# Optimization experiments

Hardware: AMD Instinct MI355X
Metric: run time of the kernel (lower is better)

The kernel has to match this reference:

```python
import jax, jax.numpy as jnp
import numpy as np

D_MODEL = 1024
NHEAD = 16
D_K = D_MODEL // NHEAD
EPS = 1e-5


def _layernorm(x, scale, bias):
    m = jnp.mean(x, axis=-1, keepdims=True)
    v = jnp.var(x, axis=-1, keepdims=True)
    return (x - m) * jax.lax.rsqrt(v + EPS) * scale + bias


def setup_inputs() -> dict:
    key = jax.random.key(0)
    ks = jax.random.split(key, 16)
    d, h = D_MODEL, 4 * D_MODEL
    s = 1.0 / np.sqrt(d)
    inp = {
        "x": jax.random.normal(ks[0], (2, 2048, d), dtype=jnp.float32),
        "Wq": jax.random.normal(ks[1], (d, d), dtype=jnp.float32) * s,
        "bq": jnp.zeros((d,), jnp.float32),
        "Wk": jax.random.normal(ks[2], (d, d), dtype=jnp.float32) * s,
        "bk": jnp.zeros((d,), jnp.float32),
        "Wv": jax.random.normal(ks[3], (d, d), dtype=jnp.float32) * s,
        "bv": jnp.zeros((d,), jnp.float32),
        "Wo": jax.random.normal(ks[4], (d, d), dtype=jnp.float32) * s,
        "bo": jnp.zeros((d,), jnp.float32),
        "ln1_scale": jnp.ones((d,), jnp.float32),
        "ln1_bias": jnp.zeros((d,), jnp.float32),
        "ln2_scale": jnp.ones((d,), jnp.float32),
        "ln2_bias": jnp.zeros((d,), jnp.float32),
        "W1": jax.random.normal(ks[5], (d, h), dtype=jnp.float32) * s,
        "b1": jnp.zeros((h,), jnp.float32),
        "W2": jax.random.normal(ks[6], (h, d), dtype=jnp.float32) * (1.0 / np.sqrt(h)),
        "b2": jnp.zeros((d,), jnp.float32),
    }
    return inp


def reference(x, Wq, bq, Wk, bk, Wv, bv, Wo, bo,
              ln1_scale, ln1_bias, ln2_scale, ln2_bias,
              W1, b1, W2, b2):
    batch, seq, d_model = x.shape
    # Faithful to original: q is viewed WITHOUT transpose (asymmetric vs k,v)
    q = (x @ Wq + bq).reshape(batch, NHEAD, seq, D_K)
    k = (x @ Wk + bk).reshape(batch, seq, NHEAD, D_K).transpose(0, 2, 1, 3)
    v = (x @ Wv + bv).reshape(batch, seq, NHEAD, D_K).transpose(0, 2, 1, 3)
    # scores: [B, H, S, S]
    scores = jnp.einsum('bhqd,bhkd->bhqk', q, k) / np.sqrt(D_K)
    attn = jax.nn.softmax(scores, axis=-1)
    o = jnp.einsum('bhqk,bhkd->bhqd', attn, v)  # [B,H,S,dk]
    o = o.transpose(0, 2, 1, 3).reshape(batch, seq, d_model)
    x = _layernorm(x + o @ Wo + bo, ln1_scale, ln1_bias)
    ff = jax.nn.relu(x @ W1 + b1) @ W2 + b2
    x = _layernorm(x + ff, ln2_scale, ln2_bias)
    return x
```

## Files before the change

### kernel.cpp

```cpp
#include <hip/hip_runtime.h>
#include <cstdint>

typedef __bf16 bf16x8 __attribute__((ext_vector_type(8)));
typedef float  floatx4 __attribute__((ext_vector_type(4)));

__device__ __forceinline__ unsigned short f2bf(float x) {
  union { float f; uint32_t u; } v; v.f = x;
  uint32_t r = (v.u + 0x7FFFu + ((v.u >> 16) & 1u)) >> 16;
  return (unsigned short)r;
}

__device__ __forceinline__ void async_copy16(const void* g, void* l) {
  __builtin_amdgcn_global_load_lds(
      (const __attribute__((address_space(1))) uint32_t*)g,
      (__attribute__((address_space(3))) uint32_t*)l, 16, 0, 0);
}

template<int OUT_BF16, int RELU>
__global__ __launch_bounds__(256, 2)
void gemm_bt_kernel(const unsigned short* __restrict__ A,
                    const unsigned short* __restrict__ Bt,
                    void* __restrict__ C, const float* __restrict__ bias,
                    int M, int N, int K, int Kper) {
  __shared__ __align__(16) unsigned short l0A[128 * 32];
  __shared__ __align__(16) unsigned short l0B[128 * 32];
  __shared__ __align__(16) unsigned short l1A[128 * 32];
  __shared__ __align__(16) unsigned short l1B[128 * 32];
  const int tid  = threadIdx.x;
  const int wave = tid >> 6;
  const int lane = tid & 63;

  const int gx = gridDim.x, gy = gridDim.y;
  int flat = blockIdx.y * gx + blockIdx.x;
  const int per = (gx * gy) >> 3;
  flat = (flat & 7) * per + (flat >> 3);
  const int sq = flat >> 6, inner = flat & 63;
  const int sqm = gy >> 3;
  const int m0 = ((sq % sqm) * 8 + (inner & 7)) * 128;
  const int n0 = ((sq / sqm) * 8 + (inner >> 3)) * 128;

  const int kz = blockIdx.z;
  const int wm = (wave >> 1) * 64;
  const int wn = (wave & 1) * 64;
  const int sa_row = lane >> 2;
  const int sa_k   = ((lane & 3) ^ ((lane >> 3) & 3)) * 8;
  const int fr = lane & 15;
  const int fq = lane >> 4;
  const int sw = (fr >> 1) & 3;

  const int r0 = (wave * 2 + 0) * 16 + sa_row;
  const int r1 = (wave * 2 + 1) * 16 + sa_row;
  const unsigned short* A0 = A  + (size_t)(m0 + r0) * K + kz * Kper + sa_k;
  const unsigned short* A1 = A  + (size_t)(m0 + r1) * K + kz * Kper + sa_k;
  const unsigned short* B0 = Bt + (size_t)(n0 + r0) * K + kz * Kper + sa_k;
  const unsigned short* B1 = Bt + (size_t)(n0 + r1) * K + kz * Kper + sa_k;

  floatx4 acc[4][4];
  #pragma unroll
  for (int i = 0; i < 4; ++i)
    #pragma unroll
    for (int j = 0; j < 4; ++j)
      acc[i][j] = (floatx4){0.f, 0.f, 0.f, 0.f};

  const int c0 = (wave * 2 + 0) * 512;
  const int c1 = (wave * 2 + 1) * 512;

#define PREFETCH(kt, LA, LB)                                   \
  do {                                                         \
    const int koff = (kt) << 5;                                \
    async_copy16(A0 + koff, &(LA)[c0]);                        \
    async_copy16(A1 + koff, &(LA)[c1]);                        \
    async_copy16(B0 + koff, &(LB)[c0]);                        \
    async_copy16(B1 + koff, &(LB)[c1]);                        \
  } while (0)

#define COMPUTE(LA, LB)                                                        \
  do {                                                                         \
    bf16x8 af[4], bf[4];                                                       \
    _Pragma("unroll")                                                          \
    for (int t = 0; t < 4; ++t) {                                              \
      af[t] = *(const bf16x8*)&(LA)[(wm + t * 16 + fr) * 32 + (fq ^ sw) * 8];  \
      bf[t] = *(const bf16x8*)&(LB)[(wn + t * 16 + fr) * 32 + (fq ^ sw) * 8];  \
    }                                                                          \
    _Pragma("unroll")                                                          \
    for (int mt = 0; mt < 4; ++mt)                                             \
      _Pragma("unroll")                                                        \
      for (int nt = 0; nt < 4; ++nt)                                           \
        acc[mt][nt] = __builtin_amdgcn_mfma_f32_16x16x32_bf16(af[mt], bf[nt],  \
                                                              acc[mt][nt], 0, 0, 0); \
  } while (0)

  const int kIters = Kper >> 5;
  PREFETCH(0, l0A, l0B);
  for (int kt = 0; kt < kIters; kt += 2) {
    PREFETCH(kt + 1, l1A, l1B);
    asm volatile("s_waitcnt vmcnt(4)" ::: "memory");
    asm volatile("s_barrier" ::: "memory");
    COMPUTE(l0A, l0B);
    asm volatile("s_barrier" ::: "memory");
    if (kt + 2 < kIters) {
      PREFETCH(kt + 2, l0A, l0B);
      asm volatile("s_waitcnt vmcnt(4)" ::: "memory");
    } else {
      asm volatile("s_waitcnt vmcnt(0)" ::: "memory");
    }
    asm volatile("s_barrier" ::: "memory");
    COMPUTE(l1A, l1B);
    asm volatile("s_barrier" ::: "memory");
  }
#undef PREFETCH
#undef COMPUTE

  const float* bp = (kz == 0) ? bias : nullptr;
  char* Cz = (char*)C + (size_t)kz * M * N * (OUT_BF16 ? 2 : 4);
  #pragma unroll
  for (int mt = 0; mt < 4; ++mt) {
    #pragma unroll
    for (int nt = 0; nt < 4; ++nt) {
      const int gn = n0 + wn + nt * 16 + fr;
      const float bv = bp ? bp[gn] : 0.f;
      #pragma unroll
      for (int r = 0; r < 4; ++r) {
        const int gm = m0 + wm + mt * 16 + fq * 4 + r;
        float v = acc[mt][nt][r] + bv;
        if (RELU) v = fmaxf(v, 0.f);
        if (OUT_BF16) ((unsigned short*)Cz)[(size_t)gm * N + gn] = f2bf(v);
        else          ((float*)Cz)[(size_t)gm * N + gn] = v;
      }
    }
  }
}

__global__ __launch_bounds__(256)
void repack_v_kernel(const unsigned short* __restrict__ X,
                     unsigned short* __restrict__ Vt) {
  const int bid = blockIdx.x;
  const int st = bid & 31, h = (bid >> 5) & 15, b = bid >> 9;
  const int bh = b * 16 + h;
  const int s0 = st * 64;
  const int t = threadIdx.x;
  const int sl = t >> 2;
  const int c  = (t & 3) * 16;
  __shared__ __align__(16) unsigned short vt[64][72];
  {
    const uint4* srcV = (const uint4*)(X + (size_t)(b * 2048 + s0 + sl) * 3072 + 2048 + h * 64 + c);
    uint4* dstL = (uint4*)&vt[sl][c];
    dstL[0] = srcV[0]; dstL[1] = srcV[1];
  }
  __syncthreads();
  const int d = t >> 2, cc = (t & 3) * 16;
  unsigned short tmp[16];
  #pragma unroll
  for (int j = 0; j < 16; ++j) {
    const int chat = cc + j;
    const int key = (chat & 3) * 16 + (chat >> 2);
    tmp[j] = vt[key][d];
  }
  uint4* dstV = (uint4*)(Vt + ((size_t)bh * 64 + d) * 2048 + s0 + cc);
  dstV[0] = *(uint4*)&tmp[0];
  dstV[1] = *(uint4*)&tmp[8];
}

__global__ __launch_bounds__(256, 4)
void flash_attn_kernel(const unsigned short* __restrict__ QKVb,
                       const unsigned short* __restrict__ Vt,
                       float* __restrict__ Opart, float* __restrict__ Lpart) {
  const int bid = blockIdx.x;
  const int qt = bid & 15, h = (bid >> 4) & 15, b = (bid >> 8) & 1, ksp = bid >> 9;
  const int bh = b * 16 + h;
  const int wave = threadIdx.x >> 6, lane = threadIdx.x & 63;
  const int fr = lane & 15, fq = lane >> 4;

  __shared__ __align__(16) unsigned short lK[64 * 64];
  __shared__ __align__(16) unsigned short lV[64 * 64];
  __shared__ __align__(16) unsigned short lP[4][32 * 72];

  const int q_base = qt * 128 + wave * 32;
  bf16x8 aq[2][2];
  #pragma unroll
  for (int g = 0; g < 2; ++g) {
    const int s2 = q_base + g * 16 + fr;
    const unsigned short* qp = QKVb + (size_t)(b * 2048 + h * 128 + (s2 >> 4)) * 3072
                             + (s2 & 15) * 64 + fq * 8;
    aq[g][0] = *(const bf16x8*)qp;
    aq[g][1] = *(const bf16x8*)(qp + 32);
  }
  floatx4 o_acc[2][4];
  #pragma unroll
  for (int g = 0; g < 2; ++g)
    #pragma unroll
    for (int nt = 0; nt < 4; ++nt) o_acc[g][nt] = (floatx4){0.f, 0.f, 0.f, 0.f};
  float lrow[2][4];
  #pragma unroll
  for (int g = 0; g < 2; ++g)
    #pragma unroll
    for (int r = 0; r < 4; ++r) lrow[g][r] = 0.f;

  const unsigned short* Kg = QKVb + 1024 + h * 64;
  const unsigned short* Vg = Vt + (size_t)bh * 64 * 2048;

  const int srow = lane >> 3;
  const int scol = ((lane & 7) ^ (lane >> 3)) * 8;
  const int sw = fr & 7;

  for (int kt = ksp * 16; kt < ksp * 16 + 16; ++kt) {
    __syncthreads();
    #pragma unroll
    for (int j = 0; j < 2; ++j) {
      const int ch = wave * 2 + j;
      const int krow = ch * 8 + srow;
      async_copy16(Kg + (size_t)(b * 2048 + kt * 64 + krow) * 3072 + scol, (char*)lK + ch * 1024);
      async_copy16(Vg + (size_t)krow * 2048 + kt * 64 + scol, (char*)lV + ch * 1024);
    }
    asm volatile("s_waitcnt vmcnt(0)" ::: "memory");
    __syncthreads();

    floatx4 s_acc[2][4];
    #pragma unroll
    for (int nt = 0; nt < 4; ++nt) {
      const int row = (nt * 16 + fr) * 64;
      bf16x8 bk0 = *(const bf16x8*)&lK[row + ((0 + fq) ^ sw) * 8];
      bf16x8 bk1 = *(const bf16x8*)&lK[row + ((4 + fq) ^ sw) * 8];
      #pragma unroll
      for (int g = 0; g < 2; ++g) {
        floatx4 acc = (floatx4){0.f, 0.f, 0.f, 0.f};
        acc = __builtin_amdgcn_mfma_f32_16x16x32_bf16(aq[g][0], bk0, acc, 0, 0, 0);
        acc = __builtin_amdgcn_mfma_f32_16x16x32_bf16(aq[g][1], bk1, acc, 0, 0, 0);
        s_acc[g][nt] = acc;
      }
    }
    #pragma unroll
    for (int g = 0; g < 2; ++g) {
      #pragma unroll
      for (int r = 0; r < 4; ++r) {
        const float p0 = __builtin_amdgcn_exp2f(s_acc[g][0][r] * 0.18033688f);
        const float p1 = __builtin_amdgcn_exp2f(s_acc[g][1][r] * 0.18033688f);
        const float p2 = __builtin_amdgcn_exp2f(s_acc[g][2][r] * 0.18033688f);
        const float p3 = __builtin_amdgcn_exp2f(s_acc[g][3][r] * 0.18033688f);
        lrow[g][r] += (p0 + p1) + (p2 + p3);
        union { float f; uint32_t u; } c0, c1, c2, c3;
        c0.f = p0; c1.f = p1; c2.f = p2; c3.f = p3;
        uint2 pk;
        pk.x = (c1.u & 0xffff0000u) | (c0.u >> 16);
        pk.y = (c3.u & 0xffff0000u) | (c2.u >> 16);
        *(uint2*)&lP[wave][(g * 16 + fq * 4 + r) * 72 + fr * 4] = pk;
      }
    }
    #pragma unroll
    for (int g = 0; g < 2; ++g) {
      #pragma unroll
      for (int kk = 0; kk < 2; ++kk) {
        bf16x8 ap = *(const bf16x8*)&lP[wave][(g * 16 + fr) * 72 + kk * 32 + fq * 8];
        #pragma unroll
        for (int nt = 0; nt < 4; ++nt) {
          bf16x8 bv = *(const bf16x8*)&lV[(nt * 16 + fr) * 64 + ((kk * 4 + fq) ^ sw) * 8];
          o_acc[g][nt] = __builtin_amdgcn_mfma_f32_16x16x32_bf16(ap, bv, o_acc[g][nt], 0, 0, 0);
        }
      }
    }
  }

  const size_t rbase = (size_t)ksp * 65536 + (size_t)bh * 2048 + q_base;
  #pragma unroll
  for (int g = 0; g < 2; ++g) {
    #pragma unroll
    for (int r = 0; r < 4; ++r) {
      float l = lrow[g][r];
      #pragma unroll
      for (int off = 1; off < 16; off <<= 1) l += __shfl_xor(l, off);
      if (fr == 0) Lpart[rbase + g * 16 + fq * 4 + r] = l;
    }
    #pragma unroll
    for (int nt = 0; nt < 4; ++nt)
      #pragma unroll
      for (int r = 0; r < 4; ++r)
        Opart[(rbase + g * 16 + fq * 4 + r) * 64 + nt * 16 + fr] = o_acc[g][nt][r];
  }
}

__global__ __launch_bounds__(256)
void attn_combine_kernel(const float* __restrict__ Opart, const float* __restrict__ Lpart,
                         unsigned short* __restrict__ O) {
  const int i = blockIdx.x * 256 + threadIdx.x;
  const int row = i >> 4;
  const int d4 = (i & 15) * 4;
  const float4 o0 = *(const float4*)&Opart[(size_t)row * 64 + d4];
  const float4 o1 = *(const float4*)&Opart[(size_t)(row + 65536) * 64 + d4];
  const float inv = 1.f / (Lpart[row] + Lpart[row + 65536]);
  const int bq = ((row >> 15) << 11) | (row & 2047);
  const int h = (row >> 11) & 15;
  ushort4 r;
  r.x = f2bf((o0.x + o1.x) * inv);
  r.y = f2bf((o0.y + o1.y) * inv);
  r.z = f2bf((o0.z + o1.z) * inv);
  r.w = f2bf((o0.w + o1.w) * inv);
  *(ushort4*)&O[(size_t)bq * 1024 + h * 64 + d4] = r;
}

__global__ __launch_bounds__(256)
void ln_kernel(const float* __restrict__ X, const float* __restrict__ R,
               const float* __restrict__ R2,
               const float* __restrict__ sc, const float* __restrict__ bi,
               float* __restrict__ outF, unsigned short* __restrict__ outB) {
  const int row = blockIdx.x;
  const int t = threadIdx.x;
  const size_t base = (size_t)row * 1024 + t * 4;
  float4 a  = *(const float4*)&X[base];
  const float4 rv = *(const float4*)&R[base];
  const float4 r2 = *(const float4*)&R2[base];
  a.x += rv.x + r2.x; a.y += rv.y + r2.y; a.z += rv.z + r2.z; a.w += rv.w + r2.w;
  float sum = (a.x + a.y) + (a.z + a.w);
  float sq  = (a.x * a.x + a.y * a.y) + (a.z * a.z + a.w * a.w);
  #pragma unroll
  for (int off = 32; off > 0; off >>= 1) {
    sum += __shfl_down(sum, off);
    sq  += __shfl_down(sq, off);
  }
  __shared__ float s1[4], s2a[4];
  const int wave = t >> 6, lane = t & 63;
  if (lane == 0) { s1[wave] = sum; s2a[wave] = sq; }
  __syncthreads();
  sum = (s1[0] + s1[1]) + (s1[2] + s1[3]);
  sq  = (s2a[0] + s2a[1]) + (s2a[2] + s2a[3]);
  const float mean = sum * (1.f / 1024.f);
  const float var  = sq * (1.f / 1024.f) - mean * mean;
  const float rstd = rsqrtf(var + 1e-5f);
  const float4 s = *(const float4*)&sc[t * 4];
  const float4 bb = *(const float4*)&bi[t * 4];
  float4 y;
  y.x = (a.x - mean) * rstd * s.x + bb.x;
  y.y = (a.y - mean) * rstd * s.y + bb.y;
  y.z = (a.z - mean) * rstd * s.z + bb.z;
  y.w = (a.w - mean) * rstd * s.w + bb.w;
  if (outF) *(float4*)&outF[base] = y;
  if (outB) {
    ushort4 ob; ob.x = f2bf(y.x); ob.y = f2bf(y.y); ob.z = f2bf(y.z); ob.w = f2bf(y.w);
    *(ushort4*)&outB[base] = ob;
  }
}

__global__ void transpose_all_kernel(const float* __restrict__ Wq, const float* __restrict__ Wk,
                                     const float* __restrict__ Wv, const float* __restrict__ Wo,
                                     const float* __restrict__ W1, const float* __restrict__ W2,
                                     unsigned short* __restrict__ Wqkvt, unsigned short* __restrict__ Wot,
                                     unsigned short* __restrict__ W1t, unsigned short* __restrict__ W2t) {
  const int id = blockIdx.x;
  const float* W; unsigned short* Wt; int K, N, tile;
  if (id < 4096) {
    const int w = id >> 10; tile = id & 1023; K = 1024; N = 1024;
    if (w == 0)      { W = Wq; Wt = Wqkvt; }
    else if (w == 1) { W = Wk; Wt = Wqkvt + 1024 * 1024; }
    else if (w == 2) { W = Wv; Wt = Wqkvt + 2048 * 1024; }
    else             { W = Wo; Wt = Wot; }
  } else if (id < 8192) { tile = id - 4096; W = W1; Wt = W1t; K = 1024; N = 4096; }
  else                  { tile = id - 8192; W = W2; Wt = W2t; K = 4096; N = 1024; }
  const int tilesX = N >> 5;
  const int bx = (tile & (tilesX - 1)) * 32;
  const int by = (tile / tilesX) * 32;
  __shared__ float tl[32][33];
  const int tx = threadIdx.x, ty = threadIdx.y;
  #pragma unroll
  for (int i = ty; i < 32; i += 8)
    tl[i][tx] = W[(size_t)(by + i) * N + bx + tx];
  __syncthreads();
  #pragma unroll
  for (int i = ty; i < 32; i += 8)
    Wt[(size_t)(bx + i) * K + by + tx] = f2bf(tl[tx][i]);
}

__global__ void cast_bf16_kernel(const float* __restrict__ in,
                                 unsigned short* __restrict__ out, int n4) {
  const int i = blockIdx.x * 256 + threadIdx.x;
  if (i < n4) {
    float4 v = ((const float4*)in)[i];
    ushort4 o;
    o.x = f2bf(v.x); o.y = f2bf(v.y); o.z = f2bf(v.z); o.w = f2bf(v.w);
    ((ushort4*)out)[i] = o;
  }
}

__global__ void concat3_kernel(const float* __restrict__ a, const float* __restrict__ b,
                               const float* __restrict__ c, float* __restrict__ out) {
  int i = blockIdx.x * 256 + threadIdx.x;
  if (i < 1024) out[i] = a[i];
  else if (i < 2048) out[i] = b[i - 1024];
  else if (i < 3072) out[i] = c[i - 2048];
}

extern "C" void kernel_launch(void* const* d_in, const int* in_sizes, int n_in,
                              void* d_out, int out_size, void* d_ws, size_t ws_size,
                              hipStream_t stream) {
  const float* x    = (const float*)d_in[0];
  const float* Wq   = (const float*)d_in[1];
  const float* bq   = (const float*)d_in[2];
  const float* Wk   = (const float*)d_in[3];
  const float* bk   = (const float*)d_in[4];
  const float* Wv   = (const float*)d_in[5];
  const float* bv   = (const float*)d_in[6];
  const float* Wo   = (const float*)d_in[7];
  const float* bo   = (const float*)d_in[8];
  const float* ln1s = (const float*)d_in[9];
  const float* ln1b = (const float*)d_in[10];
  const float* ln2s = (const float*)d_in[11];
  const float* ln2b = (const float*)d_in[12];
  const float* W1   = (const float*)d_in[13];
  const float* b1   = (const float*)d_in[14];
  const float* W2   = (const float*)d_in[15];
  const float* b2   = (const float*)d_in[16];
  float* out = (float*)d_out;

  char* ws = (char*)d_ws;
  const size_t MB = 1u << 20;
  unsigned short* QKVb = (unsigned short*)(ws + 0);
  float*          t1   = (float*)(ws + 0);
  unsigned short* ffh  = (unsigned short*)(ws + 0);
  unsigned short* Vt   = (unsigned short*)(ws + 32 * MB);
  unsigned short* Ob   = (unsigned short*)(ws + 40 * MB);
  float*          ff   = (float*)(ws + 32 * MB);
  float*          Opart= (float*)(ws + 48 * MB);
  unsigned short* xb   = (unsigned short*)(ws + 48 * MB);
  unsigned short* Wqkvt= (unsigned short*)(ws + 56 * MB);
  float*          x1   = (float*)(ws + 64 * MB);
  float*          Lpart= (float*)(ws + 80 * MB);
  unsigned short* Wot  = (unsigned short*)(ws + 81 * MB);
  unsigned short* W1t  = (unsigned short*)(ws + 83 * MB);
  unsigned short* W2t  = (unsigned short*)(ws + 91 * MB);
  float*          bqkv = (float*)(ws + 99 * MB);
  unsigned short* x1b  = (unsigned short*)(ws + 100 * MB);

  cast_bf16_kernel<<<4096, 256, 0, stream>>>(x, xb, 1048576);
  transpose_all_kernel<<<12288, dim3(32, 8), 0, stream>>>(Wq, Wk, Wv, Wo, W1, W2,
                                                          Wqkvt, Wot, W1t, W2t);
  concat3_kernel<<<12, 256, 0, stream>>>(bq, bk, bv, bqkv);

  gemm_bt_kernel<1, 0><<<dim3(24, 32, 1), 256, 0, stream>>>(xb, Wqkvt, QKVb, bqkv, 4096, 3072, 1024, 1024);
  repack_v_kernel<<<1024, 256, 0, stream>>>(QKVb, Vt);
  flash_attn_kernel<<<1024, 256, 0, stream>>>(QKVb, Vt, Opart, Lpart);
  attn_combine_kernel<<<4096, 256, 0, stream>>>(Opart, Lpart, Ob);
  gemm_bt_kernel<0, 0><<<dim3(8, 32, 2), 256, 0, stream>>>(Ob, Wot, t1, bo, 4096, 1024, 1024, 512);
  ln_kernel<<<4096, 256, 0, stream>>>(x, t1, t1 + 4096 * 1024, ln1s, ln1b, x1, x1b);
  gemm_bt_kernel<1, 1><<<dim3(32, 32, 1), 256, 0, stream>>>(x1b, W1t, ffh, b1, 4096, 4096, 1024, 1024);
  gemm_bt_kernel<0, 0><<<dim3(8, 32, 2), 256, 0, stream>>>(ffh, W2t, ff, b2, 4096, 1024, 4096, 2048);
  ln_kernel<<<4096, 256, 0, stream>>>(x1, ff, ff + 4096 * 1024, ln2s, ln2b, out, nullptr);

  (void)in_sizes; (void)n_in; (void)out_size; (void)ws_size;
}
```

Measured before the change: 362.6 us.

## Fuse attention combine into O-proj GEMM, shrink intermediates to bf16, merge prep kernels

The O-projection GEMM now loads the two bf16 split-K attention partials directly, sums them, scales by a precomputed inverse normalizer and writes bf16, which removes the separate combine kernel. Flash attention writes its partial outputs as bf16 and hoists the V fragment loads out of the inner loop. Split-K GEMM outputs and the residual input to the second layernorm are bf16 instead of fp32, and the weight-cast, x-cast and bias-concat kernels become a single prep launch. The aim is less memory traffic and fewer launches, at the cost of extra bf16 rounding on the partial sums and the residual path.

Result: no change. 362.4 us (-0.1%).

```diff
diff --git a/kernel.cpp b/kernel.cpp
--- a/kernel.cpp
+++ b/kernel.cpp
@@ -8,6 +8,15 @@
   union { float f; uint32_t u; } v; v.f = x;
   uint32_t r = (v.u + 0x7FFFu + ((v.u >> 16) & 1u)) >> 16;
   return (unsigned short)r;
+}
+__device__ __forceinline__ float bflo(uint32_t u) {
+  union { uint32_t u; float f; } v; v.u = u << 16; return v.f;
+}
+__device__ __forceinline__ float bfhi(uint32_t u) {
+  union { uint32_t u; float f; } v; v.u = u & 0xffff0000u; return v.f;
+}
+__device__ __forceinline__ float bfu(unsigned short u) {
+  union { uint32_t u; float f; } v; v.u = (uint32_t)u << 16; return v.f;
 }
 
 __device__ __forceinline__ void async_copy16(const void* g, void* l) {
@@ -131,6 +140,113 @@
   }
 }
 
+__global__ __launch_bounds__(256, 2)
+void gemm_oproj_kernel(const unsigned short* __restrict__ Opart,
+                       const float* __restrict__ invL,
+                       const unsigned short* __restrict__ Bt,
+                       unsigned short* __restrict__ C,
+                       const float* __restrict__ bias) {
+  const int K = 1024, N = 1024, M = 4096, Kper = 512;
+  __shared__ __align__(16) unsigned short lA[128 * 32];
+  __shared__ __align__(16) unsigned short lB[128 * 32];
+  const int tid  = threadIdx.x;
+  const int wave = tid >> 6;
+  const int lane = tid & 63;
+
+  const int gx = gridDim.x, gy = gridDim.y;
+  int flat = blockIdx.y * gx + blockIdx.x;
+  const int per = (gx * gy) >> 3;
+  flat = (flat & 7) * per + (flat >> 3);
+  const int sq = flat >> 6, inner = flat & 63;
+  const int sqm = gy >> 3;
+  const int m0 = ((sq % sqm) * 8 + (inner & 7)) * 128;
+  const int n0 = ((sq / sqm) * 8 + (inner >> 3)) * 128;
+
+  const int kz = blockIdx.z;
+  const int wm = (wave >> 1) * 64;
+  const int wn = (wave & 1) * 64;
+  const int sa_row = lane >> 2;
+  const int sa_k   = ((lane & 3) ^ ((lane >> 3) & 3)) * 8;
+  const int fr = lane & 15;
+  const int fq = lane >> 4;
+  const int sw = (fr >> 1) & 3;
+
+  const int r0 = (wave * 2 + 0) * 16 + sa_row;
+  const int r1 = (wave * 2 + 1) * 16 + sa_row;
+  const int gm0 = m0 + r0, gm1 = m0 + r1;
+  const int base0 = (gm0 >> 11) * 16 * 2048 + (gm0 & 2047);
+  const int base1 = (gm1 >> 11) * 16 * 2048 + (gm1 & 2047);
+  const unsigned short* B0 = Bt + (size_t)(n0 + r0) * K + kz * Kper + sa_k;
+  const unsigned short* B1 = Bt + (size_t)(n0 + r1) * K + kz * Kper + sa_k;
+  const int c0 = (wave * 2 + 0) * 512;
+  const int c1 = (wave * 2 + 1) * 512;
+
+  floatx4 acc[4][4];
+  #pragma unroll
+  for (int i = 0; i < 4; ++i)
+    #pragma unroll
+    for (int j = 0; j < 4; ++j)
+      acc[i][j] = (floatx4){0.f, 0.f, 0.f, 0.f};
+
+  for (int kt = 0; kt < 16; ++kt) {
+    __syncthreads();
+    const int kk = kz * Kper + (kt << 5) + sa_k;
+    const int h = kk >> 6, d0 = kk & 63;
+    #pragma unroll
+    for (int j = 0; j < 2; ++j) {
+      const int base = j ? base1 : base0;
+      const int cj   = j ? c1 : c0;
+      const int rowi = base + h * 2048;
+      const size_t idx = (size_t)rowi * 64 + d0;
+      const uint4 a = *(const uint4*)(Opart + idx);
+      const uint4 b = *(const uint4*)(Opart + idx + 4194304);
+      const float s = invL[rowi];
+      const uint32_t au[4] = {a.x, a.y, a.z, a.w};
+      const uint32_t bu[4] = {b.x, b.y, b.z, b.w};
+      uint32_t w[4];
+      #pragma unroll
+      for (int k = 0; k < 4; ++k) {
+        const float lo = (bflo(au[k]) + bflo(bu[k])) * s;
+        const float hi = (bfhi(au[k]) + bfhi(bu[k])) * s;
+        w[k] = (uint32_t)f2bf(lo) | ((uint32_t)f2bf(hi) << 16);
+      }
+      uint4 wv; wv.x = w[0]; wv.y = w[1]; wv.z = w[2]; wv.w = w[3];
+      *(uint4*)&lA[cj + lane * 8] = wv;
+    }
+    async_copy16(B0 + (kt << 5), &lB[c0]);
+    async_copy16(B1 + (kt << 5), &lB[c1]);
+    __syncthreads();
+
+    bf16x8 af[4], bf[4];
+    #pragma unroll
+    for (int t = 0; t < 4; ++t) {
+      af[t] = *(const bf16x8*)&lA[(wm + t * 16 + fr) * 32 + (fq ^ sw) * 8];
+      bf[t] = *(const bf16x8*)&lB[(wn + t * 16 + fr) * 32 + (fq ^ sw) * 8];
+    }
+    #pragma unroll
+    for (int mt = 0; mt < 4; ++mt)
+      #pragma unroll
+      for (int nt = 0; nt < 4; ++nt)
+        acc[mt][nt] = __builtin_amdgcn_mfma_f32_16x16x32_bf16(af[mt], bf[nt], acc[mt][nt], 0, 0, 0);
+  }
+
+  const float* bp = (kz == 0) ? bias : nullptr;
+  unsigned short* Cz = C + (size_t)kz * M * N;
+  #pragma unroll
+  for (int mt = 0; mt < 4; ++mt) {
+    #pragma unroll
+    for (int nt = 0; nt < 4; ++nt) {
+      const int gn = n0 + wn + nt * 16 + fr;
+      const float bv = bp ? bp[gn] : 0.f;
+      #pragma unroll
+      for (int r = 0; r < 4; ++r) {
+        const int gm = m0 + wm + mt * 16 + fq * 4 + r;
+        Cz[(size_t)gm * N + gn] = f2bf(acc[mt][nt][r] + bv);
+      }
+    }
+  }
+}
+
 __global__ __launch_bounds__(256)
 void repack_v_kernel(const unsigned short* __restrict__ X,
                      unsigned short* __restrict__ Vt) {
@@ -164,7 +280,7 @@
 __global__ __launch_bounds__(256, 4)
 void flash_attn_kernel(const unsigned short* __restrict__ QKVb,
                        const unsigned short* __restrict__ Vt,
-                       float* __restrict__ Opart, float* __restrict__ Lpart) {
+                       unsigned short* __restrict__ Opart, float* __restrict__ Lpart) {
   const int bid = blockIdx.x;
   const int qt = bid & 15, h = (bid >> 4) & 15, b = (bid >> 8) & 1, ksp = bid >> 9;
   const int bh = b * 16 + h;
@@ -202,16 +318,15 @@
   const int srow = lane >> 3;
   const int scol = ((lane & 7) ^ (lane >> 3)) * 8;
   const int sw = fr & 7;
+  const int ch0 = wave * 2, ch1 = wave * 2 + 1;
+  const int krow0 = ch0 * 8 + srow, krow1 = ch1 * 8 + srow;
 
   for (int kt = ksp * 16; kt < ksp * 16 + 16; ++kt) {
     __syncthreads();
-    #pragma unroll
-    for (int j = 0; j < 2; ++j) {
-      const int ch = wave * 2 + j;
-      const int krow = ch * 8 + srow;
-      async_copy16(Kg + (size_t)(b * 2048 + kt * 64 + krow) * 3072 + scol, (char*)lK + ch * 1024);
-      async_copy16(Vg + (size_t)krow * 2048 + kt * 64 + scol, (char*)lV + ch * 1024);
-    }
+    async_copy16(Kg + (size_t)(b * 2048 + kt * 64 + krow0) * 3072 + scol, (char*)lK + ch0 * 1024);
+    async_copy16(Vg + (size_t)krow0 * 2048 + kt * 64 + scol,              (char*)lV + ch0 * 1024);
+    async_copy16(Kg + (size_t)(b * 2048 + kt * 64 + krow1) * 3072 + scol, (char*)lK + ch1 * 1024);
+    async_copy16(Vg + (size_t)krow1 * 2048 + kt * 64 + scol,              (char*)lV + ch1 * 1024);
     asm volatile("s_waitcnt vmcnt(0)" ::: "memory");
     __syncthreads();
 
@@ -229,6 +344,13 @@
         s_acc[g][nt] = acc;
       }
     }
+    bf16x8 bvv[2][4];
+    #pragma unroll
+    for (int kk = 0; kk < 2; ++kk)
+      #pragma unroll
+      for (int nt = 0; nt < 4; ++nt)
+        bvv[kk][nt] = *(const bf16x8*)&lV[(nt * 16 + fr) * 64 + ((kk * 4 + fq) ^ sw) * 8];
+
     #pragma unroll
     for (int g = 0; g < 2; ++g) {
       #pragma unroll
@@ -252,10 +374,8 @@
       for (int kk = 0; kk < 2; ++kk) {
         bf16x8 ap = *(const bf16x8*)&lP[wave][(g * 16 + fr) * 72 + kk * 32 + fq * 8];
         #pragma unroll
-        for (int nt = 0; nt < 4; ++nt) {
-          bf16x8 bv = *(const bf16x8*)&lV[(nt * 16 + fr) * 64 + ((kk * 4 + fq) ^ sw) * 8];
-          o_acc[g][nt] = __builtin_amdgcn_mfma_f32_16x16x32_bf16(ap, bv, o_acc[g][nt], 0, 0, 0);
-        }
+        for (int nt = 0; nt < 4; ++nt)
+          o_acc[g][nt] = __builtin_amdgcn_mfma_f32_16x16x32_bf16(ap, bvv[kk][nt], o_acc[g][nt], 0, 0, 0);
       }
     }
   }
@@ -274,41 +394,38 @@
     for (int nt = 0; nt < 4; ++nt)
       #pragma unroll
       for (int r = 0; r < 4; ++r)
-        Opart[(rbase + g * 16 + fq * 4 + r) * 64 + nt * 16 + fr] = o_acc[g][nt][r];
+        Opart[(rbase + g * 16 + fq * 4 + r) * 64 + nt * 16 + fr] = f2bf(o_acc[g][nt][r]);
   }
 }
 
 __global__ __launch_bounds__(256)
-void attn_combine_kernel(const float* __restrict__ Opart, const float* __restrict__ Lpart,
-                         unsigned short* __restrict__ O) {
+void invl_kernel(const float* __restrict__ Lpart, float* __restrict__ invL) {
   const int i = blockIdx.x * 256 + threadIdx.x;
-  const int row = i >> 4;
-  const int d4 = (i & 15) * 4;
-  const float4 o0 = *(const float4*)&Opart[(size_t)row * 64 + d4];
-  const float4 o1 = *(const float4*)&Opart[(size_t)(row + 65536) * 64 + d4];
-  const float inv = 1.f / (Lpart[row] + Lpart[row + 65536]);
-  const int bq = ((row >> 15) << 11) | (row & 2047);
-  const int h = (row >> 11) & 15;
-  ushort4 r;
-  r.x = f2bf((o0.x + o1.x) * inv);
-  r.y = f2bf((o0.y + o1.y) * inv);
-  r.z = f2bf((o0.z + o1.z) * inv);
-  r.w = f2bf((o0.w + o1.w) * inv);
-  *(ushort4*)&O[(size_t)bq * 1024 + h * 64 + d4] = r;
-}
-
+  invL[i] = 1.f / (Lpart[i] + Lpart[i + 65536]);
+}
+
+template<int XF32, int OUTF32>
 __global__ __launch_bounds__(256)
-void ln_kernel(const float* __restrict__ X, const float* __restrict__ R,
-               const float* __restrict__ R2,
+void ln_kernel(const void* __restrict__ Xv, const unsigned short* __restrict__ R,
+               const unsigned short* __restrict__ R2,
                const float* __restrict__ sc, const float* __restrict__ bi,
                float* __restrict__ outF, unsigned short* __restrict__ outB) {
   const int row = blockIdx.x;
   const int t = threadIdx.x;
   const size_t base = (size_t)row * 1024 + t * 4;
-  float4 a  = *(const float4*)&X[base];
-  const float4 rv = *(const float4*)&R[base];
-  const float4 r2 = *(const float4*)&R2[base];
-  a.x += rv.x + r2.x; a.y += rv.y + r2.y; a.z += rv.z + r2.z; a.w += rv.w + r2.w;
+  float4 a;
+  if (XF32) {
+    a = *(const float4*)((const float*)Xv + base);
+  } else {
+    const ushort4 xu = *(const ushort4*)((const unsigned short*)Xv + base);
+    a.x = bfu(xu.x); a.y = bfu(xu.y); a.z = bfu(xu.z); a.w = bfu(xu.w);
+  }
+  const ushort4 r1u = *(const ushort4*)&R[base];
+  const ushort4 r2u = *(const ushort4*)&R2[base];
+  a.x += bfu(r1u.x) + bfu(r2u.x);
+  a.y += bfu(r1u.y) + bfu(r2u.y);
+  a.z += bfu(r1u.z) + bfu(r2u.z);
+  a.w += bfu(r1u.w) + bfu(r2u.w);
   float sum = (a.x + a.y) + (a.z + a.w);
   float sq  = (a.x * a.x + a.y * a.y) + (a.z * a.z + a.w * a.w);
   #pragma unroll
@@ -332,19 +449,39 @@
   y.y = (a.y - mean) * rstd * s.y + bb.y;
   y.z = (a.z - mean) * rstd * s.z + bb.z;
   y.w = (a.w - mean) * rstd * s.w + bb.w;
-  if (outF) *(float4*)&outF[base] = y;
-  if (outB) {
+  if (OUTF32) {
+    *(float4*)&outF[base] = y;
+  } else {
     ushort4 ob; ob.x = f2bf(y.x); ob.y = f2bf(y.y); ob.z = f2bf(y.z); ob.w = f2bf(y.w);
     *(ushort4*)&outB[base] = ob;
   }
 }
 
-__global__ void transpose_all_kernel(const float* __restrict__ Wq, const float* __restrict__ Wk,
-                                     const float* __restrict__ Wv, const float* __restrict__ Wo,
-                                     const float* __restrict__ W1, const float* __restrict__ W2,
-                                     unsigned short* __restrict__ Wqkvt, unsigned short* __restrict__ Wot,
-                                     unsigned short* __restrict__ W1t, unsigned short* __restrict__ W2t) {
+__global__ void prep_kernel(const float* __restrict__ Wq, const float* __restrict__ Wk,
+                            const float* __restrict__ Wv, const float* __restrict__ Wo,
+                            const float* __restrict__ W1, const float* __restrict__ W2,
+                            unsigned short* __restrict__ Wqkvt, unsigned short* __restrict__ Wot,
+                            unsigned short* __restrict__ W1t, unsigned short* __restrict__ W2t,
+                            const float* __restrict__ x, unsigned short* __restrict__ xb,
+                            const float* __restrict__ bq, const float* __restrict__ bk,
+                            const float* __restrict__ bv, float* __restrict__ bqkv) {
   const int id = blockIdx.x;
+  const int tflat = threadIdx.y * 32 + threadIdx.x;
+  if (id >= 16384) {
+    const int i = (id - 16384) * 256 + tflat;
+    if (i < 1024) bqkv[i] = bq[i];
+    else if (i < 2048) bqkv[i] = bk[i - 1024];
+    else if (i < 3072) bqkv[i] = bv[i - 2048];
+    return;
+  }
+  if (id >= 12288) {
+    const int i = (id - 12288) * 256 + tflat;
+    const float4 v = ((const float4*)x)[i];
+    ushort4 o;
+    o.x = f2bf(v.x); o.y = f2bf(v.y); o.z = f2bf(v.z); o.w = f2bf(v.w);
+    ((ushort4*)xb)[i] = o;
+    return;
+  }
   const float* W; unsigned short* Wt; int K, N, tile;
   if (id < 4096) {
     const int w = id >> 10; tile = id & 1023; K = 1024; N = 1024;
@@ -366,25 +503,6 @@
   #pragma unroll
   for (int i = ty; i < 32; i += 8)
     Wt[(size_t)(bx + i) * K + by + tx] = f2bf(tl[tx][i]);
-}
-
-__global__ void cast_bf16_kernel(const float* __restrict__ in,
-                                 unsigned short* __restrict__ out, int n4) {
-  const int i = blockIdx.x * 256 + threadIdx.x;
-  if (i < n4) {
-    float4 v = ((const float4*)in)[i];
-    ushort4 o;
-    o.x = f2bf(v.x); o.y = f2bf(v.y); o.z = f2bf(v.z); o.w = f2bf(v.w);
-    ((ushort4*)out)[i] = o;
-  }
-}
-
-__global__ void concat3_kernel(const float* __restrict__ a, const float* __restrict__ b,
-                               const float* __restrict__ c, float* __restrict__ out) {
-  int i = blockIdx.x * 256 + threadIdx.x;
-  if (i < 1024) out[i] = a[i];
-  else if (i < 2048) out[i] = b[i - 1024];
-  else if (i < 3072) out[i] = c[i - 2048];
 }
 
 extern "C" void kernel_launch(void* const* d_in, const int* in_sizes, int n_in,
@@ -412,36 +530,33 @@
   char* ws = (char*)d_ws;
   const size_t MB = 1u << 20;
   unsigned short* QKVb = (unsigned short*)(ws + 0);
-  float*          t1   = (float*)(ws + 0);
+  unsigned short* t1   = (unsigned short*)(ws + 0);
   unsigned short* ffh  = (unsigned short*)(ws + 0);
   unsigned short* Vt   = (unsigned short*)(ws + 32 * MB);
-  unsigned short* Ob   = (unsigned short*)(ws + 40 * MB);
-  float*          ff   = (float*)(ws + 32 * MB);
-  float*          Opart= (float*)(ws + 48 * MB);
+  unsigned short* ff   = (unsigned short*)(ws + 32 * MB);
   unsigned short* xb   = (unsigned short*)(ws + 48 * MB);
+  unsigned short* Opart= (unsigned short*)(ws + 48 * MB);
   unsigned short* Wqkvt= (unsigned short*)(ws + 56 * MB);
-  float*          x1   = (float*)(ws + 64 * MB);
   float*          Lpart= (float*)(ws + 80 * MB);
+  float*          invL = (float*)(ws + 80 * MB + 512 * 1024);
   unsigned short* Wot  = (unsigned short*)(ws + 81 * MB);
   unsigned short* W1t  = (unsigned short*)(ws + 83 * MB);
   unsigned short* W2t  = (unsigned short*)(ws + 91 * MB);
   float*          bqkv = (float*)(ws + 99 * MB);
   unsigned short* x1b  = (unsigned short*)(ws + 100 * MB);
 
-  cast_bf16_kernel<<<4096, 256, 0, stream>>>(x, xb, 1048576);
-  transpose_all_kernel<<<12288, dim3(32, 8), 0, stream>>>(Wq, Wk, Wv, Wo, W1, W2,
-                                                          Wqkvt, Wot, W1t, W2t);
-  concat3_kernel<<<12, 256, 0, stream>>>(bq, bk, bv, bqkv);
-
+  prep_kernel<<<16396, dim3(32, 8), 0, stream>>>(Wq, Wk, Wv, Wo, W1, W2,
+                                                 Wqkvt, Wot, W1t, W2t,
+                                                 x, xb, bq, bk, bv, bqkv);
   gemm_bt_kernel<1, 0><<<dim3(24, 32, 1), 256, 0, stream>>>(xb, Wqkvt, QKVb, bqkv, 4096, 3072, 1024, 1024);
   repack_v_kernel<<<1024, 256, 0, stream>>>(QKVb, Vt);
   flash_attn_kernel<<<1024, 256, 0, stream>>>(QKVb, Vt, Opart, Lpart);
-  attn_combine_kernel<<<4096, 256, 0, stream>>>(Opart, Lpart, Ob);
-  gemm_bt_kernel<0, 0><<<dim3(8, 32, 2), 256, 0, stream>>>(Ob, Wot, t1, bo, 4096, 1024, 1024, 512);
-  ln_kernel<<<4096, 256, 0, stream>>>(x, t1, t1 + 4096 * 1024, ln1s, ln1b, x1, x1b);
+  invl_kernel<<<256, 256, 0, stream>>>(Lpart, invL);
+  gemm_oproj_kernel<<<dim3(8, 32, 2), 256, 0, stream>>>(Opart, invL, Wot, t1, bo);
+  ln_kernel<1, 0><<<4096, 256, 0, stream>>>(x, t1, t1 + 4096 * 1024, ln1s, ln1b, nullptr, x1b);
   gemm_bt_kernel<1, 1><<<dim3(32, 32, 1), 256, 0, stream>>>(x1b, W1t, ffh, b1, 4096, 4096, 1024, 1024);
-  gemm_bt_kernel<0, 0><<<dim3(8, 32, 2), 256, 0, stream>>>(ffh, W2t, ff, b2, 4096, 1024, 4096, 2048);
-  ln_kernel<<<4096, 256, 0, stream>>>(x1, ff, ff + 4096 * 1024, ln2s, ln2b, out, nullptr);
+  gemm_bt_kernel<1, 0><<<dim3(8, 32, 2), 256, 0, stream>>>(ffh, W2t, ff, b2, 4096, 1024, 4096, 2048);
+  ln_kernel<0, 1><<<4096, 256, 0, stream>>>(x1b, ff, ff + 4096 * 1024, ln2s, ln2b, out, nullptr);
 
   (void)in_sizes; (void)n_in; (void)out_size; (void)ws_size;
 }
```
